# Kernel tuning notes

Measured on AMD Instinct MI355X. Metric: run time of the kernel, lower is better.

## Reference

```python
import jax, jax.numpy as jnp
import numpy as np

B, P, N, L, H = 8, 1024, 32, 125, 256
E = 3 + L  # embed_dim = 3 local coords + latent_dim
OUTPUT_BIAS = 0.5   # cfg.supervision != 'sdf'
LEVEL_SET = -0.07   # cfg.level_set
SOFT_SCALE = 100.0  # cfg.soft_transfer_scale


def setup_inputs() -> dict:
    key = jax.random.key(0)
    ks = jax.random.split(key, 12)
    rn = lambda k, s, sc=1.0: jax.random.normal(k, s, dtype=jnp.float32) * sc
    X = rn(ks[0], (B, P, 3))
    latents = rn(ks[1], (N, B, L))
    constants = jax.random.uniform(ks[2], (B, N), minval=0.5, maxval=1.5, dtype=jnp.float32)
    scales = jax.random.uniform(ks[3], (B, N, 3), minval=0.5, maxval=1.5, dtype=jnp.float32)
    rotations = rn(ks[4], (B, N, 3, 3))
    centers = rn(ks[5], (B, N, 3))
    W0 = rn(ks[6], (N, E, H), 1.0 / np.sqrt(E))
    W1 = rn(ks[7], (N, H, H), 1.0 / np.sqrt(H))
    W2 = rn(ks[8], (N, H, H), 1.0 / np.sqrt(H))
    Wout = rn(ks[9], (N, H, 1), 1.0 / np.sqrt(H))
    return dict(X=X, latents=latents, constants=constants, scales=scales,
                rotations=rotations, centers=centers,
                W0=W0, b0=jnp.zeros((N, H), jnp.float32),
                W1=W1, b1=jnp.zeros((N, H), jnp.float32),
                W2=W2, b2=jnp.zeros((N, H), jnp.float32),
                Wout=Wout, bout=jnp.zeros((N, 1), jnp.float32),
                use_constants=1)


def _forward(X, latents, constants, scales, rotations, centers,
             W0, b0, W1, b1, W2, b2, Wout, bout, use_constants):
    b, p, _ = X.shape
    n, _, l = latents.shape
    # global_to_local: rotate (X - center) into each node frame, divide by scale
    diff = X[:, :, None, :] - centers[:, None]                      # [B,P,N,3]
    local = jnp.einsum('bnij,bpnj->bpni', rotations, diff) / scales[:, None]
    # concat local coords with per-node latent broadcast over points
    lat = jnp.broadcast_to(latents.transpose(1, 0, 2)[:, None], (b, p, n, l))
    inp = jnp.concatenate([local, lat], axis=-1)                    # [B,P,N,E]
    # per-node MLP stack as batched (grouped) GEMMs over the node axis
    h = jax.nn.relu(jnp.einsum('bpne,neh->bpnh', inp, W0) + b0)
    h = jax.nn.relu(jnp.einsum('bpnh,nhk->bpnk', h, W1) + b1)
    h = jax.nn.relu(jnp.einsum('bpnh,nhk->bpnk', h, W2) + b2)
    pred_sdf = jnp.einsum('bpnh,nho->bpno', h, Wout) + bout + OUTPUT_BIAS  # [B,P,N,1]
    # sample_rbf_weights: anisotropic gaussian weight per node
    w = jnp.exp(-0.5 * jnp.sum(local * local, axis=-1))             # [B,P,N]
    if use_constants:
        w = w * constants[:, None, :]
    w = w[..., None]                                                # [B,P,N,1]
    weighted_points_sdf = w * pred_sdf
    ldif_values = jnp.sum(weighted_points_sdf, axis=2)              # [B,P,1]
    # compute_inverse_occupancy: sigmoid(soft_scale * (level_set - values))
    class_pred = jax.nn.sigmoid(SOFT_SCALE * (LEVEL_SET - ldif_values))
    return ldif_values, class_pred


def reference(X, latents, constants, scales, rotations, centers,
              W0, b0, W1, b1, W2, b2, Wout, bout, use_constants):
    return _forward(X, latents, constants, scales, rotations, centers,
                    W0, b0, W1, b1, W2, b2, Wout, bout, use_constants)
```

## Files before the change

### kernel.cpp

```cpp
#include <hip/hip_runtime.h>
#include <math.h>

#define B_ 8
#define P_ 1024
#define N_ 32
#define L_ 125
#define H_ 256
#define E_ 128
#define MT 64

static_assert(E_ == 3 + L_, "embed dim mismatch");

typedef _Float16 half8 __attribute__((ext_vector_type(8)));
typedef _Float16 half4v __attribute__((ext_vector_type(4)));
typedef float f32x16 __attribute__((ext_vector_type(16)));

__global__ void z_precompute(const float* __restrict__ latents,
                             const float* __restrict__ W0,
                             const float* __restrict__ b0,
                             float* __restrict__ Z) {
  const int n = blockIdx.x, zs = blockIdx.y;
  const int l0 = zs * 32;
  const int nl = (l0 + 32 <= L_) ? 32 : (L_ - l0);
  __shared__ float lat[B_][32];
  const int t = threadIdx.x;
  {
    const int b = t >> 5, l = t & 31;
    lat[b][l] = (l < nl) ? latents[(n * B_ + b) * L_ + l0 + l] : 0.f;
  }
  __syncthreads();
  const float* w0 = W0 + ((size_t)n * E_ + 3 + l0) * H_ + t;
  float acc[B_];
#pragma unroll
  for (int b = 0; b < B_; ++b) acc[b] = 0.f;
  for (int l = 0; l < nl; ++l) {
    const float wv = w0[(size_t)l * H_];
#pragma unroll
    for (int b = 0; b < B_; ++b) acc[b] = fmaf(lat[b][l], wv, acc[b]);
  }
  const float base = (zs == 0) ? b0[n * H_ + t] : 0.f;
#pragma unroll
  for (int b = 0; b < B_; ++b)
    atomicAdd(&Z[(b * N_ + n) * H_ + t], acc[b] + base);
}

__global__ void wsplit(const float* __restrict__ W1, const float* __restrict__ W2,
                       _Float16* __restrict__ WThi, _Float16* __restrict__ WTlo) {
  const int node = blockIdx.x;
  const int layer = blockIdx.y;
  const int jb = blockIdx.z >> 2;
  const int kb = blockIdx.z & 3;
  const float* W = (layer == 0 ? W1 : W2) + (size_t)node * H_ * H_;
  _Float16* dhi = WThi + ((size_t)layer * N_ + node) * H_ * H_;
  _Float16* dlo = WTlo + ((size_t)layer * N_ + node) * H_ * H_;
  __shared__ float tile[64][65];
  const int t = threadIdx.x;
  {
    const int col = t & 63;
#pragma unroll
    for (int i = 0; i < 16; ++i) {
      const int row = (t >> 6) * 16 + i;
      tile[row][col] = W[(size_t)(kb * 64 + row) * H_ + jb * 64 + col];
    }
  }
  __syncthreads();
  const int j_l = t >> 2;
  const int j = jb * 64 + j_l;
  const int w = j >> 5, lc = j & 31;
  const int kq = (t & 3) * 16;
  const int kc = kb * 4 + (t & 3);
  half8 hv0, hv1, lv0, lv1;
#pragma unroll
  for (int q = 0; q < 16; ++q) {
    const float v = tile[kq + q][j_l];
    const _Float16 hh = (_Float16)v;
    const _Float16 ll = (_Float16)(v - (float)hh);
    if (q < 8) { hv0[q] = hh; lv0[q] = ll; }
    else       { hv1[q - 8] = hh; lv1[q - 8] = ll; }
  }
  const size_t o0 = (size_t)w * 8192 + (size_t)kc * 512 + lc * 8;
  const size_t o1 = o0 + 256;
  *(half8*)(dhi + o0) = hv0;
  *(half8*)(dhi + o1) = hv1;
  *(half8*)(dlo + o0) = lv0;
  *(half8*)(dlo + o1) = lv1;
}

__global__ __launch_bounds__(512, 4)
void mlp_main(const float* __restrict__ X,
              const float* __restrict__ constants,
              const float* __restrict__ scales,
              const float* __restrict__ rotations,
              const float* __restrict__ centers,
              const float* __restrict__ W0,
              const float* __restrict__ b1,
              const float* __restrict__ b2,
              const float* __restrict__ Wout,
              const float* __restrict__ bout,
              const float* __restrict__ Z,
              const _Float16* __restrict__ WThi,
              const _Float16* __restrict__ WTlo,
              const int* __restrict__ use_constants,
              float* __restrict__ accum) {
  __shared__ _Float16 h_hi[MT * H_];
  __shared__ _Float16 h_lo[MT * H_];
  __shared__ float loc[MT][3];
  __shared__ float wgt[MT];
  __shared__ float predpart[MT];

  const int ell = blockIdx.x;
  const int node = (ell & 7) * 4 + ((ell >> 3) & 3);
  const int p0 = (ell >> 5) * MT;
  const int b = p0 >> 10;
  const int tid = threadIdx.x;
  const int lane = tid & 63;
  const int w = tid >> 6;
  const int lc = lane & 31;
  const int kh = lane >> 5;

  if (tid < MT) {
    predpart[tid] = 0.f;
    const int pidx = p0 + tid;
    const float x0 = X[pidx * 3 + 0];
    const float x1 = X[pidx * 3 + 1];
    const float x2 = X[pidx * 3 + 2];
    const float* R = rotations + (size_t)(b * N_ + node) * 9;
    const float* C = centers + (size_t)(b * N_ + node) * 3;
    const float* S = scales + (size_t)(b * N_ + node) * 3;
    const float d0 = x0 - C[0], d1 = x1 - C[1], d2 = x2 - C[2];
    const float l0 = (R[0] * d0 + R[1] * d1 + R[2] * d2) / S[0];
    const float l1 = (R[3] * d0 + R[4] * d1 + R[5] * d2) / S[1];
    const float l2 = (R[6] * d0 + R[7] * d1 + R[8] * d2) / S[2];
    loc[tid][0] = l0; loc[tid][1] = l1; loc[tid][2] = l2;
    float ww = expf(-0.5f * (l0 * l0 + l1 * l1 + l2 * l2));
    if (use_constants[0] != 0) ww *= constants[b * N_ + node];
    wgt[tid] = ww;
  }
  __syncthreads();

  {
    const int m = lane;
    const float l0 = loc[m][0], l1 = loc[m][1], l2 = loc[m][2];
    const float* w0p = W0 + (size_t)node * E_ * H_;
    const float* zp = Z + (size_t)(b * N_ + node) * H_;
    char* hhp = (char*)h_hi + m * 512;
    char* hlp = (char*)h_lo + m * 512;
    const int mx = m & 31;
#pragma unroll
    for (int j = w * 32; j < w * 32 + 32; j += 4) {
      const float4 a0 = *(const float4*)(w0p + j);
      const float4 a1 = *(const float4*)(w0p + H_ + j);
      const float4 a2 = *(const float4*)(w0p + 2 * H_ + j);
      const float4 zz = *(const float4*)(zp + j);
      float v[4];
      v[0] = fmaxf(fmaf(l2, a2.x, fmaf(l1, a1.x, fmaf(l0, a0.x, zz.x))), 0.f);
      v[1] = fmaxf(fmaf(l2, a2.y, fmaf(l1, a1.y, fmaf(l0, a0.y, zz.y))), 0.f);
      v[2] = fmaxf(fmaf(l2, a2.z, fmaf(l1, a1.z, fmaf(l0, a0.z, zz.z))), 0.f);
      v[3] = fmaxf(fmaf(l2, a2.w, fmaf(l1, a1.w, fmaf(l0, a0.w, zz.w))), 0.f);
      half4v hv, lv;
#pragma unroll
      for (int r = 0; r < 4; ++r) {
        const _Float16 h16 = (_Float16)v[r];
        hv[r] = h16;
        lv[r] = (_Float16)(v[r] - (float)h16);
      }
      const int off = (((j >> 3) ^ mx) << 4) + ((j & 7) << 1);
      *(half4v*)(hhp + off) = hv;
      *(half4v*)(hlp + off) = lv;
    }
  }
  __syncthreads();

  f32x16 acc0, acc1;

  const size_t wb = (size_t)node * H_ * H_ + (size_t)w * 8192 + (kh * 32 + lc) * 8;
  const _Float16* wt1hi = WThi + wb;
  const _Float16* wt1lo = WTlo + wb;
  const _Float16* wt2hi = WThi + (size_t)N_ * H_ * H_ + wb;
  const _Float16* wt2lo = WTlo + (size_t)N_ * H_ * H_ + wb;

  const char* rbh0 = (const char*)h_hi + lc * 512;
  const char* rbh1 = (const char*)h_hi + (32 + lc) * 512;
  const char* rbl0 = (const char*)h_lo + lc * 512;
  const char* rbl1 = (const char*)h_lo + (32 + lc) * 512;

  auto run_layer = [&](const _Float16* __restrict__ wh,
                       const _Float16* __restrict__ wl) {
    acc0 = (f32x16)(0.f);
    acc1 = (f32x16)(0.f);
    half8 aH = *(const half8*)(wh);
    half8 aL = *(const half8*)(wl);
#pragma unroll
    for (int kc = 0; kc < 16; ++kc) {
      half8 aHn, aLn;
      if (kc < 15) {
        aHn = *(const half8*)(wh + (kc + 1) * 512);
        aLn = *(const half8*)(wl + (kc + 1) * 512);
      }
      const int so = ((2 * kc + kh) ^ lc) << 4;
      const half8 bh0 = *(const half8*)(rbh0 + so);
      const half8 bh1 = *(const half8*)(rbh1 + so);
      const half8 bl0 = *(const half8*)(rbl0 + so);
      const half8 bl1 = *(const half8*)(rbl1 + so);
      __builtin_amdgcn_s_setprio(1);
      acc0 = __builtin_amdgcn_mfma_f32_32x32x16_f16(aH, bh0, acc0, 0, 0, 0);
      acc0 = __builtin_amdgcn_mfma_f32_32x32x16_f16(aH, bl0, acc0, 0, 0, 0);
      acc0 = __builtin_amdgcn_mfma_f32_32x32x16_f16(aL, bh0, acc0, 0, 0, 0);
      acc1 = __builtin_amdgcn_mfma_f32_32x32x16_f16(aH, bh1, acc1, 0, 0, 0);
      acc1 = __builtin_amdgcn_mfma_f32_32x32x16_f16(aH, bl1, acc1, 0, 0, 0);
      acc1 = __builtin_amdgcn_mfma_f32_32x32x16_f16(aL, bh1, acc1, 0, 0, 0);
      __builtin_amdgcn_s_setprio(0);
      if (kc < 15) { aH = aHn; aL = aLn; }
    }
  };

  run_layer(wt1hi, wt1lo);
  __syncthreads();
  {
#pragma unroll
    for (int q = 0; q < 4; ++q) {
      const int jq = 32 * w + 8 * q + 4 * kh;
      const float4 bb = *(const float4*)(b1 + node * H_ + jq);
      const float bv[4] = {bb.x, bb.y, bb.z, bb.w};
      const int soff = ((((4 * w + q) ^ lc) << 4) + (kh << 3));
      half4v hv, lv;
#pragma unroll
      for (int r = 0; r < 4; ++r) {
        const float v = fmaxf(acc0[4 * q + r] + bv[r], 0.f);
        const _Float16 h16 = (_Float16)v;
        hv[r] = h16;
        lv[r] = (_Float16)(v - (float)h16);
      }
      *(half4v*)((char*)h_hi + lc * 512 + soff) = hv;
      *(half4v*)((char*)h_lo + lc * 512 + soff) = lv;
#pragma unroll
      for (int r = 0; r < 4; ++r) {
        const float v = fmaxf(acc1[4 * q + r] + bv[r], 0.f);
        const _Float16 h16 = (_Float16)v;
        hv[r] = h16;
        lv[r] = (_Float16)(v - (float)h16);
      }
      *(half4v*)((char*)h_hi + (32 + lc) * 512 + soff) = hv;
      *(half4v*)((char*)h_lo + (32 + lc) * 512 + soff) = lv;
    }
  }
  __syncthreads();

  run_layer(wt2hi, wt2lo);
  {
    float s0 = 0.f, s1 = 0.f;
#pragma unroll
    for (int q = 0; q < 4; ++q) {
      const int jq = 32 * w + 8 * q + 4 * kh;
      const float4 bb = *(const float4*)(b2 + node * H_ + jq);
      const float4 wo = *(const float4*)(Wout + node * H_ + jq);
      const float bv[4] = {bb.x, bb.y, bb.z, bb.w};
      const float wv[4] = {wo.x, wo.y, wo.z, wo.w};
#pragma unroll
      for (int r = 0; r < 4; ++r) {
        s0 = fmaf(fmaxf(acc0[4 * q + r] + bv[r], 0.f), wv[r], s0);
        s1 = fmaf(fmaxf(acc1[4 * q + r] + bv[r], 0.f), wv[r], s1);
      }
    }
    s0 += __shfl_xor(s0, 32, 64);
    s1 += __shfl_xor(s1, 32, 64);
    if (lane < 32) {
      atomicAdd(&predpart[lc], s0);
      atomicAdd(&predpart[32 + lc], s1);
    }
  }
  __syncthreads();

  if (tid < MT)
    atomicAdd(&accum[p0 + tid], wgt[tid] * (predpart[tid] + bout[node] + 0.5f));
}

__global__ void finalize(const float* __restrict__ accum, float* __restrict__ out) {
  const int i = blockIdx.x * 256 + threadIdx.x;
  const float v = accum[i];
  out[i] = v;
  const float zz = 100.0f * (-0.07f - v);
  out[B_ * P_ + i] = 1.0f / (1.0f + expf(-zz));
}

extern "C" void kernel_launch(void* const* d_in, const int* in_sizes, int n_in,
                              void* d_out, int out_size, void* d_ws, size_t ws_size,
                              hipStream_t stream) {
  const float* X = (const float*)d_in[0];
  const float* latents = (const float*)d_in[1];
  const float* constants = (const float*)d_in[2];
  const float* scales = (const float*)d_in[3];
  const float* rotations = (const float*)d_in[4];
  const float* centers = (const float*)d_in[5];
  const float* W0 = (const float*)d_in[6];
  const float* b0 = (const float*)d_in[7];
  const float* W1 = (const float*)d_in[8];
  const float* b1 = (const float*)d_in[9];
  const float* W2 = (const float*)d_in[10];
  const float* b2 = (const float*)d_in[11];
  const float* Wout = (const float*)d_in[12];
  const float* bout = (const float*)d_in[13];
  const int* use_constants = (const int*)d_in[14];

  float* accum = (float*)d_ws;
  float* Zbuf = accum + B_ * P_;
  _Float16* WThi = (_Float16*)(Zbuf + B_ * N_ * H_);
  _Float16* WTlo = WThi + (size_t)2 * N_ * H_ * H_;

  hipMemsetAsync(accum, 0, (B_ * P_ + B_ * N_ * H_) * sizeof(float), stream);

  z_precompute<<<dim3(N_, 4), 256, 0, stream>>>(latents, W0, b0, Zbuf);
  wsplit<<<dim3(N_, 2, 16), 256, 0, stream>>>(W1, W2, WThi, WTlo);

  mlp_main<<<dim3(B_ * P_ / MT * N_), 512, 0, stream>>>(
      X, constants, scales, rotations, centers, W0, b1, b2, Wout, bout,
      Zbuf, WThi, WTlo, use_constants, accum);

  finalize<<<dim3(B_ * P_ / 256), 256, 0, stream>>>(accum, (float*)d_out);
}
```

Baseline: 287.7 us.

## Fuse prep kernels, pipeline MFMA operand loads, replace atomics with per-node buffer

Merges the Z precompute and weight-split kernels into one launch. Z is now computed without atomics, so the memset can be dropped. The MFMA inner loop now double-buffers LDS B operands, prefetches global A operands two steps ahead, and interleaves the acc0/acc1 MFMAs to break dependency chains. The final atomic accumulation is replaced by per-node writes to a [N,B*P] buffer that finalize sums, trading atomics for extra memory traffic and register pressure.

```diff
diff --git a/kernel.cpp b/kernel.cpp
--- a/kernel.cpp
+++ b/kernel.cpp
@@ -15,75 +15,67 @@
 typedef _Float16 half4v __attribute__((ext_vector_type(4)));
 typedef float f32x16 __attribute__((ext_vector_type(16)));
 
-__global__ void z_precompute(const float* __restrict__ latents,
-                             const float* __restrict__ W0,
-                             const float* __restrict__ b0,
-                             float* __restrict__ Z) {
-  const int n = blockIdx.x, zs = blockIdx.y;
-  const int l0 = zs * 32;
-  const int nl = (l0 + 32 <= L_) ? 32 : (L_ - l0);
-  __shared__ float lat[B_][32];
+__global__ void prep(const float* __restrict__ latents,
+                     const float* __restrict__ W0,
+                     const float* __restrict__ b0,
+                     const float* __restrict__ W1,
+                     const float* __restrict__ W2,
+                     float* __restrict__ Z,
+                     _Float16* __restrict__ WThi,
+                     _Float16* __restrict__ WTlo) {
+  const int bid = blockIdx.x;
   const int t = threadIdx.x;
-  {
-    const int b = t >> 5, l = t & 31;
-    lat[b][l] = (l < nl) ? latents[(n * B_ + b) * L_ + l0 + l] : 0.f;
-  }
-  __syncthreads();
-  const float* w0 = W0 + ((size_t)n * E_ + 3 + l0) * H_ + t;
-  float acc[B_];
-#pragma unroll
-  for (int b = 0; b < B_; ++b) acc[b] = 0.f;
-  for (int l = 0; l < nl; ++l) {
-    const float wv = w0[(size_t)l * H_];
-#pragma unroll
-    for (int b = 0; b < B_; ++b) acc[b] = fmaf(lat[b][l], wv, acc[b]);
-  }
-  const float base = (zs == 0) ? b0[n * H_ + t] : 0.f;
-#pragma unroll
-  for (int b = 0; b < B_; ++b)
-    atomicAdd(&Z[(b * N_ + n) * H_ + t], acc[b] + base);
-}
-
-__global__ void wsplit(const float* __restrict__ W1, const float* __restrict__ W2,
-                       _Float16* __restrict__ WThi, _Float16* __restrict__ WTlo) {
-  const int node = blockIdx.x;
-  const int layer = blockIdx.y;
-  const int jb = blockIdx.z >> 2;
-  const int kb = blockIdx.z & 3;
-  const float* W = (layer == 0 ? W1 : W2) + (size_t)node * H_ * H_;
-  _Float16* dhi = WThi + ((size_t)layer * N_ + node) * H_ * H_;
-  _Float16* dlo = WTlo + ((size_t)layer * N_ + node) * H_ * H_;
-  __shared__ float tile[64][65];
-  const int t = threadIdx.x;
-  {
-    const int col = t & 63;
-#pragma unroll
-    for (int i = 0; i < 16; ++i) {
-      const int row = (t >> 6) * 16 + i;
-      tile[row][col] = W[(size_t)(kb * 64 + row) * H_ + jb * 64 + col];
-    }
-  }
-  __syncthreads();
-  const int j_l = t >> 2;
-  const int j = jb * 64 + j_l;
-  const int w = j >> 5, lc = j & 31;
-  const int kq = (t & 3) * 16;
-  const int kc = kb * 4 + (t & 3);
-  half8 hv0, hv1, lv0, lv1;
-#pragma unroll
-  for (int q = 0; q < 16; ++q) {
-    const float v = tile[kq + q][j_l];
-    const _Float16 hh = (_Float16)v;
-    const _Float16 ll = (_Float16)(v - (float)hh);
-    if (q < 8) { hv0[q] = hh; lv0[q] = ll; }
-    else       { hv1[q - 8] = hh; lv1[q - 8] = ll; }
-  }
-  const size_t o0 = (size_t)w * 8192 + (size_t)kc * 512 + lc * 8;
-  const size_t o1 = o0 + 256;
-  *(half8*)(dhi + o0) = hv0;
-  *(half8*)(dhi + o1) = hv1;
-  *(half8*)(dlo + o0) = lv0;
-  *(half8*)(dlo + o1) = lv1;
+  if (bid < N_ * B_) {
+    __shared__ float lat[L_];
+    const int n = bid >> 3, b = bid & 7;
+    if (t < L_) lat[t] = latents[(n * B_ + b) * L_ + t];
+    __syncthreads();
+    const float* w0 = W0 + ((size_t)n * E_ + 3) * H_ + t;
+    float acc = b0[n * H_ + t];
+#pragma unroll 5
+    for (int l = 0; l < L_; ++l)
+      acc = fmaf(lat[l], w0[(size_t)l * H_], acc);
+    Z[(b * N_ + n) * H_ + t] = acc;
+  } else {
+    const int id = bid - N_ * B_;
+    const int node = id >> 5;
+    const int layer = (id >> 4) & 1;
+    const int jb = (id >> 2) & 3;
+    const int kb = id & 3;
+    const float* W = (layer == 0 ? W1 : W2) + (size_t)node * H_ * H_;
+    _Float16* dhi = WThi + ((size_t)layer * N_ + node) * H_ * H_;
+    _Float16* dlo = WTlo + ((size_t)layer * N_ + node) * H_ * H_;
+    __shared__ float tile[64][65];
+    {
+      const int col = t & 63;
+#pragma unroll
+      for (int i = 0; i < 16; ++i) {
+        const int row = (t >> 6) * 16 + i;
+        tile[row][col] = W[(size_t)(kb * 64 + row) * H_ + jb * 64 + col];
+      }
+    }
+    __syncthreads();
+    const int j_l = t >> 2;
+    const int j = jb * 64 + j_l;
+    const int w = j >> 5, lc = j & 31;
+    const int kq = (t & 3) * 16;
+    const int kc = kb * 4 + (t & 3);
+    half8 hv0, hv1, lv0, lv1;
+#pragma unroll
+    for (int q = 0; q < 16; ++q) {
+      const float v = tile[kq + q][j_l];
+      const _Float16 hh = (_Float16)v;
+      const _Float16 ll = (_Float16)(v - (float)hh);
+      if (q < 8) { hv0[q] = hh; lv0[q] = ll; }
+      else       { hv1[q - 8] = hh; lv1[q - 8] = ll; }
+    }
+    const size_t o0 = (size_t)w * 8192 + (size_t)kc * 512 + lc * 8;
+    const size_t o1 = o0 + 256;
+    *(half8*)(dhi + o0) = hv0;
+    *(half8*)(dhi + o1) = hv1;
+    *(half8*)(dlo + o0) = lv0;
+    *(half8*)(dlo + o1) = lv1;
+  }
 }
 
 __global__ __launch_bounds__(512, 4)
@@ -101,7 +93,7 @@
               const _Float16* __restrict__ WThi,
               const _Float16* __restrict__ WTlo,
               const int* __restrict__ use_constants,
-              float* __restrict__ accum) {
+              float* __restrict__ pred) {
   __shared__ _Float16 h_hi[MT * H_];
   __shared__ _Float16 h_lo[MT * H_];
   __shared__ float loc[MT][3];
@@ -188,29 +180,42 @@
                        const _Float16* __restrict__ wl) {
     acc0 = (f32x16)(0.f);
     acc1 = (f32x16)(0.f);
-    half8 aH = *(const half8*)(wh);
-    half8 aL = *(const half8*)(wl);
+    half8 aH[3], aL[3];
+    half8 bh0[2], bh1[2], bl0[2], bl1[2];
+    aH[0] = *(const half8*)(wh);
+    aL[0] = *(const half8*)(wl);
+    aH[1] = *(const half8*)(wh + 512);
+    aL[1] = *(const half8*)(wl + 512);
+    {
+      const int so = (kh ^ lc) << 4;
+      bh0[0] = *(const half8*)(rbh0 + so);
+      bh1[0] = *(const half8*)(rbh1 + so);
+      bl0[0] = *(const half8*)(rbl0 + so);
+      bl1[0] = *(const half8*)(rbl1 + so);
+    }
 #pragma unroll
     for (int kc = 0; kc < 16; ++kc) {
-      half8 aHn, aLn;
+      const int cur = kc & 1, nxt = cur ^ 1;
+      const int ac = kc % 3, a2 = (kc + 2) % 3;
+      if (kc < 14) {
+        aH[a2] = *(const half8*)(wh + (kc + 2) * 512);
+        aL[a2] = *(const half8*)(wl + (kc + 2) * 512);
+      }
       if (kc < 15) {
-        aHn = *(const half8*)(wh + (kc + 1) * 512);
-        aLn = *(const half8*)(wl + (kc + 1) * 512);
-      }
-      const int so = ((2 * kc + kh) ^ lc) << 4;
-      const half8 bh0 = *(const half8*)(rbh0 + so);
-      const half8 bh1 = *(const half8*)(rbh1 + so);
-      const half8 bl0 = *(const half8*)(rbl0 + so);
-      const half8 bl1 = *(const half8*)(rbl1 + so);
+        const int so = ((2 * (kc + 1) + kh) ^ lc) << 4;
+        bh0[nxt] = *(const half8*)(rbh0 + so);
+        bh1[nxt] = *(const half8*)(rbh1 + so);
+        bl0[nxt] = *(const half8*)(rbl0 + so);
+        bl1[nxt] = *(const half8*)(rbl1 + so);
+      }
       __builtin_amdgcn_s_setprio(1);
-      acc0 = __builtin_amdgcn_mfma_f32_32x32x16_f16(aH, bh0, acc0, 0, 0, 0);
-      acc0 = __builtin_amdgcn_mfma_f32_32x32x16_f16(aH, bl0, acc0, 0, 0, 0);
-      acc0 = __builtin_amdgcn_mfma_f32_32x32x16_f16(aL, bh0, acc0, 0, 0, 0);
-      acc1 = __builtin_amdgcn_mfma_f32_32x32x16_f16(aH, bh1, acc1, 0, 0, 0);
-      acc1 = __builtin_amdgcn_mfma_f32_32x32x16_f16(aH, bl1, acc1, 0, 0, 0);
-      acc1 = __builtin_amdgcn_mfma_f32_32x32x16_f16(aL, bh1, acc1, 0, 0, 0);
+      acc0 = __builtin_amdgcn_mfma_f32_32x32x16_f16(aH[ac], bh0[cur], acc0, 0, 0, 0);
+      acc1 = __builtin_amdgcn_mfma_f32_32x32x16_f16(aH[ac], bh1[cur], acc1, 0, 0, 0);
+      acc0 = __builtin_amdgcn_mfma_f32_32x32x16_f16(aH[ac], bl0[cur], acc0, 0, 0, 0);
+      acc1 = __builtin_amdgcn_mfma_f32_32x32x16_f16(aH[ac], bl1[cur], acc1, 0, 0, 0);
+      acc0 = __builtin_amdgcn_mfma_f32_32x32x16_f16(aL[ac], bh0[cur], acc0, 0, 0, 0);
+      acc1 = __builtin_amdgcn_mfma_f32_32x32x16_f16(aL[ac], bh1[cur], acc1, 0, 0, 0);
       __builtin_amdgcn_s_setprio(0);
-      if (kc < 15) { aH = aHn; aL = aLn; }
     }
   };
 
@@ -272,12 +277,15 @@
   __syncthreads();
 
   if (tid < MT)
-    atomicAdd(&accum[p0 + tid], wgt[tid] * (predpart[tid] + bout[node] + 0.5f));
+    pred[(size_t)node * (B_ * P_) + p0 + tid] =
+        wgt[tid] * (predpart[tid] + bout[node] + 0.5f);
 }
 
-__global__ void finalize(const float* __restrict__ accum, float* __restrict__ out) {
+__global__ void finalize(const float* __restrict__ pred, float* __restrict__ out) {
   const int i = blockIdx.x * 256 + threadIdx.x;
-  const float v = accum[i];
+  float v = 0.f;
+#pragma unroll
+  for (int n = 0; n < N_; ++n) v += pred[n * (B_ * P_) + i];
   out[i] = v;
   const float zz = 100.0f * (-0.07f - v);
   out[B_ * P_ + i] = 1.0f / (1.0f + expf(-zz));
@@ -302,19 +310,17 @@
   const float* bout = (const float*)d_in[13];
   const int* use_constants = (const int*)d_in[14];
 
-  float* accum = (float*)d_ws;
-  float* Zbuf = accum + B_ * P_;
+  float* pred = (float*)d_ws;
+  float* Zbuf = pred + (size_t)N_ * B_ * P_;
   _Float16* WThi = (_Float16*)(Zbuf + B_ * N_ * H_);
   _Float16* WTlo = WThi + (size_t)2 * N_ * H_ * H_;
 
-  hipMemsetAsync(accum, 0, (B_ * P_ + B_ * N_ * H_) * sizeof(float), stream);
-
-  z_precompute<<<dim3(N_, 4), 256, 0, stream>>>(latents, W0, b0, Zbuf);
-  wsplit<<<dim3(N_, 2, 16), 256, 0, stream>>>(W1, W2, WThi, WTlo);
+  prep<<<dim3(N_ * B_ + N_ * 2 * 16), 256, 0, stream>>>(
+      latents, W0, b0, W1, W2, Zbuf, WThi, WTlo);
 
   mlp_main<<<dim3(B_ * P_ / MT * N_), 512, 0, stream>>>(
       X, constants, scales, rotations, centers, W0, b1, b2, Wout, bout,
-      Zbuf, WThi, WTlo, use_constants, accum);
-
-  finalize<<<dim3(B_ * P_ / 256), 256, 0, stream>>>(accum, (float*)d_out);
+      Zbuf, WThi, WTlo, use_constants, pred);
+
+  finalize<<<dim3(B_ * P_ / 256), 256, 0, stream>>>(pred, (float*)d_out);
 }
```

After: 299.0 us. +3.9%, slower.
